# Kernel optimization log

Measured on AMD Instinct MI355X. Metric: run time of the kernel, lower is better.

The kernel has to match this reference:

```python
import jax, jax.numpy as jnp
import numpy as np

DIM = 384
HEADS = 8
HD = DIM // HEADS
GAMMA = 0.5
EPS = 1e-6
BN_EPS = 1e-5
LN_EPS = 1e-5


def setup_inputs() -> dict:
    key = jax.random.key(0)
    ks = jax.random.split(key, 8)
    B, H, W = 8, 56, 56
    d = DIM
    w = lambda k, shp: (jax.random.normal(k, shp, jnp.float32) * 0.05)
    return {
        "x": jax.random.normal(ks[0], (B, d, H, W), jnp.float32),
        "bn1_w": jnp.ones((d,), jnp.float32), "bn1_b": jnp.zeros((d,), jnp.float32),
        "bn1_m": jnp.zeros((d,), jnp.float32), "bn1_v": jnp.ones((d,), jnp.float32),
        "cw1": w(ks[1], (d, d)), "cb1": jnp.zeros((d,), jnp.float32),
        "dw": w(ks[2], (d, 1, 3, 3)), "db": jnp.zeros((d,), jnp.float32),
        "bn2_w": jnp.ones((d,), jnp.float32), "bn2_b": jnp.zeros((d,), jnp.float32),
        "bn2_m": jnp.zeros((d,), jnp.float32), "bn2_v": jnp.ones((d,), jnp.float32),
        "cw2": w(ks[3], (d, d)), "cb2": jnp.zeros((d,), jnp.float32),
        "qkv_w": w(ks[4], (3 * d, d)),
        "proj_w": w(ks[5], (d, d)), "proj_b": jnp.zeros((d,), jnp.float32),
        "ln_w": jnp.ones((d,), jnp.float32), "ln_b": jnp.zeros((d,), jnp.float32),
        "mlp_w1": w(ks[6], (d, 4 * d)), "mlp_b1": jnp.zeros((4 * d,), jnp.float32),
        "mlp_w2": w(ks[7], (4 * d, d)), "mlp_b2": jnp.zeros((d,), jnp.float32),
    }


def _bn(t, w, b, m, v):
    # inference-mode BatchNorm2d over channel dim of NCHW
    s = w * jax.lax.rsqrt(v + BN_EPS)
    return (t - m[:, None, None]) * s[:, None, None] + b[:, None, None]


def _c1(t, w, b=None):
    # 1x1 conv as channel GEMM: (o,i) x (b,i,h,w) -> (b,o,h,w)
    y = jnp.einsum('oi,bihw->bohw', w, t)
    return y if b is None else y + b[:, None, None]


def _phi(t):
    return jnp.exp(GAMMA * (2.0 * t - t * t))


def reference(x, bn1_w, bn1_b, bn1_m, bn1_v, cw1, cb1, dw, db,
              bn2_w, bn2_b, bn2_m, bn2_v, cw2, cb2, qkv_w,
              proj_w, proj_b, ln_w, ln_b, mlp_w1, mlp_b1, mlp_w2, mlp_b2):
    B, C, H, W = x.shape
    N = H * W
    # conv_path with residual
    h = _bn(x, bn1_w, bn1_b, bn1_m, bn1_v)
    h = _c1(h, cw1, cb1)
    h = jax.lax.conv_general_dilated(h, dw, (1, 1), 'SAME',
                                     feature_group_count=DIM,
                                     dimension_numbers=('NCHW', 'OIHW', 'NCHW'))
    h = h + db[:, None, None]
    h = _bn(h, bn2_w, bn2_b, bn2_m, bn2_v)
    h = _c1(h, cw2, cb2)
    x1 = h + x
    # linear attention
    qkv = _c1(x1, qkv_w)  # (B, 3C, H, W)
    q, k, v = jnp.split(qkv, 3, axis=1)
    to_heads = lambda t: t.reshape(B, HEADS, HD, N).transpose(0, 1, 3, 2)  # (B,h,N,d)
    qp = _phi(to_heads(q))
    kp = _phi(to_heads(k))
    vv = to_heads(v)
    kv = jnp.einsum('bhnd,bhne->bhde', kp, vv)               # (B,h,d,d)
    z = 1.0 / (jnp.einsum('bhnd,bhd->bhn', qp, kp.sum(axis=2)) + EPS)
    out = jnp.einsum('bhnd,bhde->bhne', qp, kv) * z[..., None]  # (B,h,N,d)
    out = out.transpose(0, 1, 3, 2).reshape(B, C, H, W)
    out = _c1(out, proj_w, proj_b)
    x2 = x1 + out
    # LayerNorm + MLP over channels
    xf = x2.transpose(0, 2, 3, 1)  # (B,H,W,C)
    mu = xf.mean(-1, keepdims=True)
    var = xf.var(-1, keepdims=True)
    xn = (xf - mu) * jax.lax.rsqrt(var + LN_EPS) * ln_w + ln_b
    hmid = jax.nn.gelu(xn @ mlp_w1 + mlp_b1, approximate=False)
    mlp_out = hmid @ mlp_w2 + mlp_b2
    return x2 + mlp_out.transpose(0, 3, 1, 2)
```

## Files before the change

### kernel.cpp

```cpp
#include <hip/hip_runtime.h>

#define CDIM 384
#define NPIX 3136
#define BB 8
#define NROW (BB * NPIX)
#define HDIM 48
#define CMID 1536
#define BN_EPS 1e-5f
#define LN_EPS 1e-5f

typedef short s16x8 __attribute__((ext_vector_type(8)));
typedef float f32x4 __attribute__((ext_vector_type(4)));
typedef unsigned short u16;

__device__ __forceinline__ u16 f2bf(float f) {
    unsigned u = __builtin_bit_cast(unsigned, f);
    u = (u + 0x7FFFu + ((u >> 16) & 1u)) >> 16;
    return (u16)u;
}
__device__ __forceinline__ float bf2f(u16 h) {
    unsigned u = ((unsigned)h) << 16;
    return __builtin_bit_cast(float, u);
}
__device__ __forceinline__ float phi_act(float v) { return expf(0.5f * (2.f * v - v * v)); }
__device__ __forceinline__ float gelu_act(float v) { return 0.5f * v * (1.f + erff(v * 0.7071067811865476f)); }

#define GLL16(g, l) __builtin_amdgcn_global_load_lds( \
    (const __attribute__((address_space(1))) void*)(g), \
    (__attribute__((address_space(3))) void*)(l), 16, 0, 0)

template<int ACT, bool BIAS, bool RES, bool OBF, bool OF32, int TN, bool QKV>
__global__ __launch_bounds__(256) void gemm_mfma(
    const u16* __restrict__ A, const u16* __restrict__ Bw,
    u16* __restrict__ Cbf, u16* __restrict__ Cv, float* __restrict__ Cf,
    const float* __restrict__ res, const float* __restrict__ bias,
    int N, int K)
{
    constexpr int NFR = TN / 32;
    constexpr int TNw = TN / 2;
    constexpr int STR = TNw + 4;
    constexpr int KLOOP_U16 = 8192 + TN * 64;
    constexpr int STG_U16 = 4 * 64 * STR;
    constexpr int SMEM_N = KLOOP_U16 > STG_U16 ? KLOOP_U16 : STG_U16;
    __shared__ __align__(16) u16 smem[SMEM_N];
    u16* Asb = smem;
    u16* Bsb = smem + 8192;

    const int t  = threadIdx.x;
    const int wv = t >> 6, ln = t & 63;
    const int lm = ln & 15, lq = ln >> 4;
    const int wm = wv >> 1, wn = wv & 1;
    const int m0 = blockIdx.y << 7, n0 = blockIdx.x * TN;

    const u16* gA0 = A  + (long)(m0 + wv * 16 + lm) * K + lq * 8;
    const u16* gA1 = gA0 + (long)64 * K;
    const u16* gB0 = Bw + (long)(n0 + wv * 16 + lm) * K + lq * 8;
    const u16* gB1 = gB0 + (long)64 * K;

    f32x4 acc[4][NFR] = {};
    const int nk = K >> 5;

    GLL16(gA0, &Asb[wv * 512]);
    GLL16(gA1, &Asb[wv * 512 + 2048]);
    GLL16(gB0, &Bsb[wv * 512]);
    if constexpr (TN == 128) GLL16(gB1, &Bsb[wv * 512 + 2048]);

    for (int k = 0; k < nk; k++) {
        const int cur = k & 1;
        __syncthreads();
        if (k + 1 < nk) {
            const int nx = cur ^ 1;
            gA0 += 32; gA1 += 32; gB0 += 32;
            GLL16(gA0, &Asb[nx * 4096 + wv * 512]);
            GLL16(gA1, &Asb[nx * 4096 + wv * 512 + 2048]);
            GLL16(gB0, &Bsb[nx * TN * 32 + wv * 512]);
            if constexpr (TN == 128) { gB1 += 32; GLL16(gB1, &Bsb[nx * TN * 32 + wv * 512 + 2048]); }
        }
        s16x8 av[4], bv[NFR];
        #pragma unroll
        for (int mf = 0; mf < 4; mf++)
            av[mf] = *(const s16x8*)&Asb[cur * 4096 + (wm * 256 + mf * 64 + ln) * 8];
        #pragma unroll
        for (int nf = 0; nf < NFR; nf++)
            bv[nf] = *(const s16x8*)&Bsb[cur * TN * 32 + ((TN == 128 ? wn * 256 : wn * 128) + nf * 64 + ln) * 8];
        #pragma unroll
        for (int mf = 0; mf < 4; mf++)
            #pragma unroll
            for (int nf = 0; nf < NFR; nf++)
                acc[mf][nf] = __builtin_amdgcn_mfma_f32_16x16x32_bf16(
                    av[mf], bv[nf], acc[mf][nf], 0, 0, 0);
    }

    u16* obase = Cbf; int oldc = N; int ocol0 = n0;
    bool qk_phi = false;
    if constexpr (QKV) {
        if (n0 < 768) { obase = Cbf; oldc = 768; ocol0 = n0; qk_phi = true; }
        else          { obase = Cv;  oldc = 384; ocol0 = n0 - 768; }
    }

    if constexpr (OBF || QKV) {
        __syncthreads();
        u16* stg = smem + wv * (64 * STR);
        #pragma unroll
        for (int nf = 0; nf < NFR; nf++) {
            const int lc = nf * 16 + lm;
            const int gn = n0 + wn * TNw + lc;
            const float bval = BIAS ? bias[gn] : 0.f;
            #pragma unroll
            for (int mf = 0; mf < 4; mf++) {
                #pragma unroll
                for (int r = 0; r < 4; r++) {
                    const int lr = mf * 16 + lq * 4 + r;
                    float v = acc[mf][nf][r];
                    if (BIAS) v += bval;
                    if (ACT == 1) v = phi_act(v);
                    else if (ACT == 2) v = gelu_act(v);
                    if (QKV) { if (qk_phi) v = phi_act(v); }
                    const long off = (long)(m0 + wm * 64 + lr) * N + gn;
                    if (RES) v += res[off];
                    if (OF32) Cf[off] = v;
                    stg[lr * STR + lc] = f2bf(v);
                }
            }
        }
        __syncthreads();
        constexpr int CPR = TNw / 8;
        constexpr int RPI = 64 / CPR;
        const int cg = ln % CPR, rb = ln / CPR;
        #pragma unroll
        for (int it = 0; it < 64 / RPI; it++) {
            const int row = it * RPI + rb;
            const s16x8 vv = *(const s16x8*)&stg[row * STR + cg * 8];
            *(s16x8*)&obase[(long)(m0 + wm * 64 + row) * oldc + ocol0 + wn * TNw + cg * 8] = vv;
        }
    } else {
        #pragma unroll
        for (int nf = 0; nf < NFR; nf++) {
            const int gn = n0 + wn * TNw + nf * 16 + lm;
            const float bval = BIAS ? bias[gn] : 0.f;
            #pragma unroll
            for (int mf = 0; mf < 4; mf++) {
                const int gmb = m0 + wm * 64 + mf * 16 + lq * 4;
                #pragma unroll
                for (int r = 0; r < 4; r++) {
                    float v = acc[mf][nf][r];
                    if (BIAS) v += bval;
                    if (ACT == 1) v = phi_act(v);
                    else if (ACT == 2) v = gelu_act(v);
                    const long off = (long)(gmb + r) * N + gn;
                    if (RES) v += res[off];
                    Cf[off] = v;
                }
            }
        }
    }
}

__global__ __launch_bounds__(256) void nchw_to_nhwc(const float* __restrict__ x,
                                                    float* __restrict__ of,
                                                    u16* __restrict__ ob)
{
    __shared__ float tile[64 * 65];
    const int n0 = blockIdx.x << 6, c0 = blockIdx.y << 6, b = blockIdx.z;
    const int t = threadIdx.x;
    const float* ip = x + ((long)b * CDIM + c0) * NPIX + n0;
    for (int idx = t; idx < 4096; idx += 256) {
        const int cc = idx >> 6, nn = idx & 63;
        tile[cc * 65 + nn] = ip[(long)cc * NPIX + nn];
    }
    __syncthreads();
    for (int idx = t; idx < 4096; idx += 256) {
        const int nn = idx >> 6, cc = idx & 63;
        const float v = tile[cc * 65 + nn];
        const long o = ((long)b * NPIX + n0 + nn) * CDIM + c0 + cc;
        of[o] = v; ob[o] = f2bf(v);
    }
}

__global__ __launch_bounds__(256) void dwconv_nhwc(const u16* __restrict__ in,
                                                   const u16* __restrict__ wt,
                                                   u16* __restrict__ out)
{
    const long tid = (long)blockIdx.x * 256 + threadIdx.x;
    const int c8 = (int)(tid % 48);
    const int p  = (int)((tid / 48) % NPIX);
    const int b  = (int)(tid / (48LL * NPIX));
    const int y = p / 56, x = p % 56;
    const u16* base = in + (long)b * NPIX * CDIM + c8 * 8;
    float acc[8] = {};
    #pragma unroll
    for (int r = 0; r < 3; r++) {
        const int yy = y + r - 1;
        if ((unsigned)yy >= 56u) continue;
        #pragma unroll
        for (int s = 0; s < 3; s++) {
            const int xx = x + s - 1;
            if ((unsigned)xx >= 56u) continue;
            const s16x8 iv = *(const s16x8*)&base[(long)(yy * 56 + xx) * CDIM];
            const s16x8 wv = *(const s16x8*)&wt[(r * 3 + s) * CDIM + c8 * 8];
            #pragma unroll
            for (int j = 0; j < 8; j++)
                acc[j] = fmaf(bf2f((u16)iv[j]), bf2f((u16)wv[j]), acc[j]);
        }
    }
    s16x8 ov;
    #pragma unroll
    for (int j = 0; j < 8; j++) ov[j] = (short)f2bf(acc[j]);
    *(s16x8*)&out[((long)b * NPIX + p) * CDIM + c8 * 8] = ov;
}

__global__ __launch_bounds__(256) void attn_kv_m(const u16* __restrict__ qk,
                                                 const u16* __restrict__ vb,
                                                 float* __restrict__ kv,
                                                 float* __restrict__ ksum)
{
    const int sp = blockIdx.x, bh = blockIdx.y;
    const int b = bh >> 3, h = bh & 7;
    const u16* kbase = qk + (long)b * NPIX * 768 + 384 + h * HDIM;
    const u16* vbase = vb + (long)b * NPIX * CDIM + h * HDIM;
    __shared__ u16 kt[48 * 72];
    __shared__ u16 vt[48 * 72];
    const int t = threadIdx.x;
    const int wv = t >> 6, ln = t & 63, lm = ln & 15, lq = ln >> 4;

    f32x4 acc[3] = {};
    const s16x8 ones = {0x3F80, 0x3F80, 0x3F80, 0x3F80, 0x3F80, 0x3F80, 0x3F80, 0x3F80};

    for (int tl = sp; tl < 49; tl += 8) {
        const int nn0 = tl << 6;
        __syncthreads();
        for (int idx = t; idx < 384; idx += 256) {
            const int oct = idx >> 6, nn = idx & 63;
            const s16x8 kvv = *(const s16x8*)&kbase[(long)(nn0 + nn) * 768 + oct * 8];
            const s16x8 vvv = *(const s16x8*)&vbase[(long)(nn0 + nn) * CDIM + oct * 8];
            #pragma unroll
            for (int j = 0; j < 8; j++) {
                kt[(oct * 8 + j) * 72 + nn] = (u16)kvv[j];
                vt[(oct * 8 + j) * 72 + nn] = (u16)vvv[j];
            }
        }
        __syncthreads();
        #pragma unroll
        for (int s = 0; s < 2; s++) {
            if (wv < 3) {
                const s16x8 av = *(const s16x8*)&kt[(wv * 16 + lm) * 72 + s * 32 + lq * 8];
                #pragma unroll
                for (int ef = 0; ef < 3; ef++) {
                    const s16x8 bv = *(const s16x8*)&vt[(ef * 16 + lm) * 72 + s * 32 + lq * 8];
                    acc[ef] = __builtin_amdgcn_mfma_f32_16x16x32_bf16(av, bv, acc[ef], 0, 0, 0);
                }
            } else {
                #pragma unroll
                for (int mf = 0; mf < 3; mf++) {
                    const s16x8 av = *(const s16x8*)&kt[(mf * 16 + lm) * 72 + s * 32 + lq * 8];
                    acc[mf] = __builtin_amdgcn_mfma_f32_16x16x32_bf16(av, ones, acc[mf], 0, 0, 0);
                }
            }
        }
    }
    if (wv < 3) {
        #pragma unroll
        for (int ef = 0; ef < 3; ef++)
            #pragma unroll
            for (int r = 0; r < 4; r++)
                atomicAdd(&kv[(long)bh * 2304 + (wv * 16 + lq * 4 + r) * 48 + ef * 16 + lm], acc[ef][r]);
    } else {
        if (lm == 0) {
            #pragma unroll
            for (int mf = 0; mf < 3; mf++)
                #pragma unroll
                for (int r = 0; r < 4; r++)
                    atomicAdd(&ksum[bh * 48 + mf * 16 + lq * 4 + r], acc[mf][r]);
        }
    }
}

__global__ void repack_kv(const float* __restrict__ kvb, const float* __restrict__ ksb,
                          u16* __restrict__ kvp, u16* __restrict__ ksp)
{
    const int bh = blockIdx.x, t = threadIdx.x;
    for (int idx = t; idx < 3072; idx += 256) {
        const int e = idx >> 6, d = idx & 63;
        kvp[(long)bh * 3072 + idx] = (d < 48) ? f2bf(kvb[(long)bh * 2304 + d * 48 + e]) : (u16)0;
    }
    if (t < 64) ksp[bh * 64 + t] = (t < 48) ? f2bf(ksb[bh * 48 + t]) : (u16)0;
}

__global__ __launch_bounds__(256) void attn_out_m(const u16* __restrict__ qk,
                                                  const u16* __restrict__ kvp,
                                                  const u16* __restrict__ ksp,
                                                  u16* __restrict__ outb)
{
    __shared__ __align__(16) u16 smem[4 * 7168];
    const int mt = blockIdx.x, hh = blockIdx.y, b = blockIdx.z;
    const int t = threadIdx.x, wv = t >> 6, ln = t & 63, lm = ln & 15, lq = ln >> 4;
    const int h = hh * 4 + wv, bh = b * 8 + h;
    u16* As = smem + wv * 7168;
    u16* Bs = As + 4096;
    const u16* Ab = qk + ((long)b * NPIX + mt * 64) * 768 + h * HDIM;
    const u16* Bb = kvp + (long)bh * 3072;

    #pragma unroll
    for (int rg = 0; rg < 4; rg++)
        #pragma unroll
        for (int oh = 0; oh < 2; oh++)
            GLL16(Ab + (long)(rg * 16 + lm) * 768 + oh * 32 + lq * 8, As + (rg * 128 + oh * 64) * 8);
    #pragma unroll
    for (int rg = 0; rg < 3; rg++)
        #pragma unroll
        for (int oh = 0; oh < 2; oh++)
            GLL16(Bb + (rg * 16 + lm) * 64 + oh * 32 + lq * 8, Bs + (rg * 128 + oh * 64) * 8);

    s16x8 kz[2];
    kz[0] = *(const s16x8*)&ksp[bh * 64 + lq * 8];
    kz[1] = *(const s16x8*)&ksp[bh * 64 + 32 + lq * 8];

    __syncthreads();

    f32x4 acc[4][3] = {};
    f32x4 accz[4] = {};
    #pragma unroll
    for (int s = 0; s < 2; s++) {
        s16x8 av[4], bv[3];
        #pragma unroll
        for (int mf = 0; mf < 4; mf++)
            av[mf] = *(const s16x8*)&As[(mf * 128 + s * 64 + ln) * 8];
        #pragma unroll
        for (int nf = 0; nf < 3; nf++)
            bv[nf] = *(const s16x8*)&Bs[(nf * 128 + s * 64 + ln) * 8];
        #pragma unroll
        for (int mf = 0; mf < 4; mf++) {
            #pragma unroll
            for (int nf = 0; nf < 3; nf++)
                acc[mf][nf] = __builtin_amdgcn_mfma_f32_16x16x32_bf16(av[mf], bv[nf], acc[mf][nf], 0, 0, 0);
            accz[mf] = __builtin_amdgcn_mfma_f32_16x16x32_bf16(av[mf], kz[s], accz[mf], 0, 0, 0);
        }
    }

    u16* stg = As;
    #pragma unroll
    for (int mf = 0; mf < 4; mf++) {
        #pragma unroll
        for (int r = 0; r < 4; r++) {
            const float z = 1.f / (accz[mf][r] + 1e-6f);
            const int row = mf * 16 + lq * 4 + r;
            #pragma unroll
            for (int nf = 0; nf < 3; nf++)
                stg[row * 56 + nf * 16 + lm] = f2bf(acc[mf][nf][r] * z);
        }
    }
    __syncthreads();

    #pragma unroll
    for (int it = 0; it < 6; it++) {
        const int idx = it * 256 + t;
        const int row = idx / 24, c = idx % 24;
        const int sw = c / 6, c6 = c % 6;
        const s16x8 vvv = *(const s16x8*)&smem[sw * 7168 + row * 56 + c6 * 8];
        *(s16x8*)&outb[((long)b * NPIX + mt * 64 + row) * CDIM + hh * 192 + c * 8] = vvv;
    }
}

__global__ __launch_bounds__(256) void ln_k(const float* __restrict__ x2,
                                            const float* __restrict__ lw,
                                            const float* __restrict__ lb,
                                            u16* __restrict__ xn)
{
    const int row = blockIdx.x * 4 + (threadIdx.x >> 6);
    const int lane = threadIdx.x & 63;
    const float* rp = x2 + (long)row * CDIM;
    float2 v[3];
    float sum = 0.f, sq = 0.f;
    #pragma unroll
    for (int i = 0; i < 3; i++) {
        v[i] = *(const float2*)&rp[lane * 2 + i * 128];
        sum += v[i].x + v[i].y;
        sq = fmaf(v[i].x, v[i].x, fmaf(v[i].y, v[i].y, sq));
    }
    #pragma unroll
    for (int off = 1; off < 64; off <<= 1) {
        sum += __shfl_xor(sum, off);
        sq  += __shfl_xor(sq, off);
    }
    const float mu = sum * (1.f / CDIM);
    const float rs = rsqrtf(sq * (1.f / CDIM) - mu * mu + LN_EPS);
    u16* op = xn + (long)row * CDIM;
    #pragma unroll
    for (int i = 0; i < 3; i++) {
        const int c = lane * 2 + i * 128;
        op[c]     = f2bf((v[i].x - mu) * rs * lw[c] + lb[c]);
        op[c + 1] = f2bf((v[i].y - mu) * rs * lw[c + 1] + lb[c + 1]);
    }
}

__global__ __launch_bounds__(256) void final_out(const float* __restrict__ x2,
                                                 const float* __restrict__ mlp,
                                                 float* __restrict__ out)
{
    __shared__ float tile[64 * 65];
    const int n0 = blockIdx.x << 6, c0 = blockIdx.y << 6, b = blockIdx.z;
    const int t = threadIdx.x;
    for (int idx = t; idx < 4096; idx += 256) {
        const int nn = idx >> 6, cc = idx & 63;
        const long o = ((long)b * NPIX + n0 + nn) * CDIM + c0 + cc;
        tile[nn * 65 + cc] = x2[o] + mlp[o];
    }
    __syncthreads();
    float* op = out + ((long)b * CDIM + c0) * NPIX + n0;
    for (int idx = t; idx < 4096; idx += 256) {
        const int cc = idx >> 6, nn = idx & 63;
        op[(long)cc * NPIX + nn] = tile[nn * 65 + cc];
    }
}

__global__ void prep_bn_k(const float* __restrict__ w1, const float* __restrict__ b1,
                          const float* __restrict__ m1, const float* __restrict__ v1,
                          const float* __restrict__ w2, const float* __restrict__ b2,
                          const float* __restrict__ m2, const float* __restrict__ v2,
                          const float* __restrict__ db,
                          float* s1, float* t1, float* s2, float* t2)
{
    const int i = threadIdx.x;
    if (i < CDIM) {
        const float a = w1[i] * rsqrtf(v1[i] + BN_EPS);
        s1[i] = a; t1[i] = b1[i] - m1[i] * a;
        const float c = w2[i] * rsqrtf(v2[i] + BN_EPS);
        s2[i] = c; t2[i] = b2[i] - m2[i] * c + db[i] * c;
    }
}

__global__ __launch_bounds__(64) void prep_w_k(
    const float* __restrict__ cw1, const float* __restrict__ cb1,
    const float* __restrict__ cw2, const float* __restrict__ cb2,
    const float* __restrict__ s1, const float* __restrict__ t1,
    const float* __restrict__ s2, const float* __restrict__ t2,
    u16* __restrict__ w1e, float* __restrict__ b1e,
    u16* __restrict__ w2e, float* __restrict__ b2e)
{
    const int o = blockIdx.x;
    const bool sec = (o >= CDIM);
    const int oo = sec ? o - CDIM : o;
    const float* cw = sec ? cw2 : cw1;
    const float* cb = sec ? cb2 : cb1;
    const float* s  = sec ? s2  : s1;
    const float* tt = sec ? t2  : t1;
    u16* we = sec ? w2e : w1e;
    float* be = sec ? b2e : b1e;
    float part = 0.f;
    for (int i = threadIdx.x; i < CDIM; i += 64) {
        const float wv = cw[oo * CDIM + i];
        we[oo * CDIM + i] = f2bf(wv * s[i]);
        part += wv * tt[i];
    }
    for (int off = 32; off; off >>= 1) part += __shfl_down(part, off);
    if (threadIdx.x == 0) be[oo] = cb[oo] + part;
}

__global__ void cvt_k(const float* __restrict__ in, u16* __restrict__ out, int n)
{
    const int i = blockIdx.x * 256 + threadIdx.x;
    if (i < n) out[i] = f2bf(in[i]);
}

__global__ __launch_bounds__(256) void transcvt_k(const float* __restrict__ in,
                                                  u16* __restrict__ out, int R, int C)
{
    __shared__ float tile[64 * 65];
    const int c0 = blockIdx.x << 6, r0 = blockIdx.y << 6;
    const int t = threadIdx.x;
    for (int idx = t; idx < 4096; idx += 256) {
        const int rr = idx >> 6, cc = idx & 63;
        tile[rr * 65 + cc] = in[(long)(r0 + rr) * C + c0 + cc];
    }
    __syncthreads();
    for (int idx = t; idx < 4096; idx += 256) {
        const int cc = idx >> 6, rr = idx & 63;
        out[(long)(c0 + cc) * R + r0 + rr] = f2bf(tile[rr * 65 + cc]);
    }
}

__global__ void dwt_k(const float* __restrict__ dw, u16* __restrict__ o)
{
    const int i = blockIdx.x * 256 + threadIdx.x;
    if (i < 9 * CDIM) {
        const int c = i / 9, tap = i % 9;
        o[tap * CDIM + c] = f2bf(dw[i]);
    }
}

extern "C" void kernel_launch(void* const* d_in, const int* in_sizes, int n_in,
                              void* d_out, int out_size, void* d_ws, size_t ws_size,
                              hipStream_t stream)
{
    const float* x      = (const float*)d_in[0];
    const float* bn1_w  = (const float*)d_in[1];
    const float* bn1_b  = (const float*)d_in[2];
    const float* bn1_m  = (const float*)d_in[3];
    const float* bn1_v  = (const float*)d_in[4];
    const float* cw1    = (const float*)d_in[5];
    const float* cb1    = (const float*)d_in[6];
    const float* dwW    = (const float*)d_in[7];
    const float* db     = (const float*)d_in[8];
    const float* bn2_w  = (const float*)d_in[9];
    const float* bn2_b  = (const float*)d_in[10];
    const float* bn2_m  = (const float*)d_in[11];
    const float* bn2_v  = (const float*)d_in[12];
    const float* cw2    = (const float*)d_in[13];
    const float* cb2    = (const float*)d_in[14];
    const float* qkv_w  = (const float*)d_in[15];
    const float* proj_w = (const float*)d_in[16];
    const float* proj_b = (const float*)d_in[17];
    const float* ln_w   = (const float*)d_in[18];
    const float* ln_b   = (const float*)d_in[19];
    const float* mlp_w1 = (const float*)d_in[20];
    const float* mlp_b1 = (const float*)d_in[21];
    const float* mlp_w2 = (const float*)d_in[22];
    const float* mlp_b2 = (const float*)d_in[23];
    float* outF = (float*)d_out;

    const long S = (long)NROW * CDIM;
    float* wsf = (float*)d_ws;

    float* xh_f  = wsf;
    float* x2_f  = wsf;
    u16*   v_bf  = (u16*)wsf;
    float* x1_f  = wsf + S;
    u16*   hmid  = (u16*)(wsf + S);
    u16* ar   = (u16*)(wsf + 2 * S);
    u16* a0   = ar;
    u16* a1   = ar + S;
    u16* a2   = ar + 2 * S;
    float* mlp_f = (float*)(ar + S);
    u16* wtb   = (u16*)(wsf + 3 * S + S / 2);
    u16* w1e   = wtb;
    u16* w2e   = w1e + CDIM * CDIM;
    u16* qkvw  = w2e + CDIM * CDIM;
    u16* projw = qkvw + 1152 * CDIM;
    u16* mw1t  = projw + CDIM * CDIM;
    u16* mw2t  = mw1t + CMID * CDIM;
    u16* dwt   = mw2t + CDIM * CMID;
    float* fb  = (float*)(dwt + 9 * CDIM);
    float* b1e = fb;
    float* b2e = b1e + CDIM;
    float* s1  = b2e + CDIM;
    float* t1  = s1 + CDIM;
    float* s2  = t1 + CDIM;
    float* t2  = s2 + CDIM;
    float* kvb = t2 + CDIM;
    float* ksb = kvb + 64 * HDIM * HDIM;
    u16*   kvp = (u16*)(ksb + 64 * HDIM);
    u16*   ksp = kvp + 64 * 3072;

    prep_bn_k<<<1, CDIM, 0, stream>>>(bn1_w, bn1_b, bn1_m, bn1_v,
                                      bn2_w, bn2_b, bn2_m, bn2_v, db, s1, t1, s2, t2);
    prep_w_k<<<2 * CDIM, 64, 0, stream>>>(cw1, cb1, cw2, cb2, s1, t1, s2, t2,
                                          w1e, b1e, w2e, b2e);
    cvt_k<<<(1152 * CDIM + 255) / 256, 256, 0, stream>>>(qkv_w, qkvw, 1152 * CDIM);
    cvt_k<<<(CDIM * CDIM + 255) / 256, 256, 0, stream>>>(proj_w, projw, CDIM * CDIM);
    transcvt_k<<<dim3(CMID / 64, CDIM / 64), 256, 0, stream>>>(mlp_w1, mw1t, CDIM, CMID);
    transcvt_k<<<dim3(CDIM / 64, CMID / 64), 256, 0, stream>>>(mlp_w2, mw2t, CMID, CDIM);
    dwt_k<<<(9 * CDIM + 255) / 256, 256, 0, stream>>>(dwW, dwt);

    nchw_to_nhwc<<<dim3(49, 6, 8), 256, 0, stream>>>(x, xh_f, a0);
    gemm_mfma<0, true, false, true, false, 64, false><<<dim3(6, 196), 256, 0, stream>>>(
        a0, w1e, a1, nullptr, nullptr, nullptr, b1e, CDIM, CDIM);
    dwconv_nhwc<<<(int)((long)BB * NPIX * 48 / 256), 256, 0, stream>>>(a1, dwt, a2);
    gemm_mfma<0, true, true, true, true, 64, false><<<dim3(6, 196), 256, 0, stream>>>(
        a2, w2e, a0, nullptr, x1_f, xh_f, b2e, CDIM, CDIM);
    gemm_mfma<0, false, false, true, false, 128, true><<<dim3(9, 196), 256, 0, stream>>>(
        a0, qkvw, a1, v_bf, nullptr, nullptr, nullptr, 1152, CDIM);
    hipMemsetAsync(kvb, 0, (size_t)(64 * HDIM * HDIM + 64 * HDIM) * sizeof(float), stream);
    attn_kv_m<<<dim3(8, 64), 256, 0, stream>>>(a1, v_bf, kvb, ksb);
    repack_kv<<<64, 256, 0, stream>>>(kvb, ksb, kvp, ksp);
    attn_out_m<<<dim3(49, 2, 8), 256, 0, stream>>>(a1, kvp, ksp, a0);
    gemm_mfma<0, true, true, false, true, 64, false><<<dim3(6, 196), 256, 0, stream>>>(
        a0, projw, nullptr, nullptr, x2_f, x1_f, proj_b, CDIM, CDIM);
    ln_k<<<NROW / 4, 256, 0, stream>>>(x2_f, ln_w, ln_b, a0);
    const long RH = (long)NROW / 2;
    gemm_mfma<2, true, false, true, false, 128, false><<<dim3(12, 98), 256, 0, stream>>>(
        a0, mw1t, hmid, nullptr, nullptr, nullptr, mlp_b1, CMID, CDIM);
    gemm_mfma<0, true, false, false, true, 64, false><<<dim3(6, 98), 256, 0, stream>>>(
        hmid, mw2t, nullptr, nullptr, mlp_f, nullptr, mlp_b2, CDIM, CMID);
    gemm_mfma<2, true, false, true, false, 128, false><<<dim3(12, 98), 256, 0, stream>>>(
        a0 + RH * CDIM, mw1t, hmid, nullptr, nullptr, nullptr, mlp_b1, CMID, CDIM);
    gemm_mfma<0, true, false, false, true, 64, false><<<dim3(6, 98), 256, 0, stream>>>(
        hmid, mw2t, nullptr, nullptr, mlp_f + RH * CDIM, nullptr, mlp_b2, CDIM, CMID);
    final_out<<<dim3(49, 6, 8), 256, 0, stream>>>(x2_f, mlp_f, outF);
}
```

Baseline: 623.5 us.

## Fuse final NCHW transpose into MLP GEMM epilogue and drop fp32 input copy

The second MLP GEMM now adds the x2 residual itself and writes straight into the NCHW output through an LDS-staged transpose, which removes the separate final_out kernel and the fp32 mlp intermediate buffer. The input conversion no longer writes an fp32 NHWC copy of x. The conv-path residual now reads the bf16 copy of x, which lowers the precision of that residual add. A block-index remap also groups consecutive tiles onto the same XCD to improve cache locality.

```diff
diff --git a/kernel.cpp b/kernel.cpp
--- a/kernel.cpp
+++ b/kernel.cpp
@@ -29,28 +29,37 @@
     (const __attribute__((address_space(1))) void*)(g), \
     (__attribute__((address_space(3))) void*)(l), 16, 0, 0)
 
-template<int ACT, bool BIAS, bool RES, bool OBF, bool OF32, int TN, bool QKV>
+template<int ACT, bool BIAS, int RES, bool OBF, bool OF32, bool ONCHW, int TN, bool QKV>
 __global__ __launch_bounds__(256) void gemm_mfma(
     const u16* __restrict__ A, const u16* __restrict__ Bw,
     u16* __restrict__ Cbf, u16* __restrict__ Cv, float* __restrict__ Cf,
-    const float* __restrict__ res, const float* __restrict__ bias,
-    int N, int K)
+    const void* __restrict__ resv, const float* __restrict__ bias,
+    int N, int K, long mrow0)
 {
     constexpr int NFR = TN / 32;
     constexpr int TNw = TN / 2;
     constexpr int STR = TNw + 4;
     constexpr int KLOOP_U16 = 8192 + TN * 64;
     constexpr int STG_U16 = 4 * 64 * STR;
-    constexpr int SMEM_N = KLOOP_U16 > STG_U16 ? KLOOP_U16 : STG_U16;
+    constexpr int ONCHW_U16 = ONCHW ? (64 * 132 * 2) : 0;
+    constexpr int SMEM_A = KLOOP_U16 > STG_U16 ? KLOOP_U16 : STG_U16;
+    constexpr int SMEM_N = SMEM_A > ONCHW_U16 ? SMEM_A : ONCHW_U16;
     __shared__ __align__(16) u16 smem[SMEM_N];
     u16* Asb = smem;
     u16* Bsb = smem + 8192;
+
+    const int total = gridDim.x * gridDim.y;
+    const int flat = blockIdx.y * gridDim.x + blockIdx.x;
+    const int nx8 = total >> 3, rem = total & 7;
+    const int xcd = flat & 7, slot = flat >> 3;
+    const int nf2 = xcd * nx8 + (xcd < rem ? xcd : rem) + slot;
+    const int by = nf2 / gridDim.x, bx = nf2 - by * gridDim.x;
 
     const int t  = threadIdx.x;
     const int wv = t >> 6, ln = t & 63;
     const int lm = ln & 15, lq = ln >> 4;
     const int wm = wv >> 1, wn = wv & 1;
-    const int m0 = blockIdx.y << 7, n0 = blockIdx.x * TN;
+    const int m0 = by << 7, n0 = bx * TN;
 
     const u16* gA0 = A  + (long)(m0 + wv * 16 + lm) * K + lq * 8;
     const u16* gA1 = gA0 + (long)64 * K;
@@ -117,7 +126,8 @@
                     else if (ACT == 2) v = gelu_act(v);
                     if (QKV) { if (qk_phi) v = phi_act(v); }
                     const long off = (long)(m0 + wm * 64 + lr) * N + gn;
-                    if (RES) v += res[off];
+                    if (RES == 1) v += ((const float*)resv)[off];
+                    else if (RES == 2) v += bf2f(((const u16*)resv)[off]);
                     if (OF32) Cf[off] = v;
                     stg[lr * STR + lc] = f2bf(v);
                 }
@@ -132,6 +142,44 @@
             const int row = it * RPI + rb;
             const s16x8 vv = *(const s16x8*)&stg[row * STR + cg * 8];
             *(s16x8*)&obase[(long)(m0 + wm * 64 + row) * oldc + ocol0 + wn * TNw + cg * 8] = vv;
+        }
+    } else if constexpr (ONCHW) {
+        __syncthreads();
+        float* stgf = (float*)smem;
+        const float* resf = (const float*)resv;
+        #pragma unroll
+        for (int nf = 0; nf < NFR; nf++) {
+            const int lc = nf * 16 + lm;
+            const int col = wn * TNw + lc;
+            const int gn = n0 + col;
+            const float bval = BIAS ? bias[gn] : 0.f;
+            #pragma unroll
+            for (int mf = 0; mf < 4; mf++) {
+                float4 q;
+                float* qq = (float*)&q;
+                #pragma unroll
+                for (int r = 0; r < 4; r++) {
+                    const int lr = mf * 16 + lq * 4 + r;
+                    float v = acc[mf][nf][r];
+                    if (BIAS) v += bval;
+                    if (ACT == 1) v = phi_act(v);
+                    else if (ACT == 2) v = gelu_act(v);
+                    if (RES == 1) v += resf[(long)(m0 + wm * 64 + lr) * N + gn];
+                    qq[r] = v;
+                }
+                *(float4*)&stgf[col * 132 + wm * 64 + mf * 16 + lq * 4] = q;
+            }
+        }
+        __syncthreads();
+        #pragma unroll
+        for (int it = 0; it < 8; it++) {
+            const int c = it * 8 + (t >> 5);
+            const int mloc = (t & 31) * 4;
+            const float4 vv = *(const float4*)&stgf[c * 132 + mloc];
+            const long mg = mrow0 + m0 + mloc;
+            const int b = (int)(mg / NPIX);
+            const int n = (int)(mg % NPIX);
+            *(float4*)&Cf[((long)b * CDIM + n0 + c) * NPIX + n] = vv;
         }
     } else {
         #pragma unroll
@@ -148,7 +196,8 @@
                     if (ACT == 1) v = phi_act(v);
                     else if (ACT == 2) v = gelu_act(v);
                     const long off = (long)(gmb + r) * N + gn;
-                    if (RES) v += res[off];
+                    if (RES == 1) v += ((const float*)resv)[off];
+                    else if (RES == 2) v += bf2f(((const u16*)resv)[off]);
                     Cf[off] = v;
                 }
             }
@@ -156,9 +205,8 @@
     }
 }
 
-__global__ __launch_bounds__(256) void nchw_to_nhwc(const float* __restrict__ x,
-                                                    float* __restrict__ of,
-                                                    u16* __restrict__ ob)
+__global__ __launch_bounds__(256) void nchw_to_bf(const float* __restrict__ x,
+                                                  u16* __restrict__ ob)
 {
     __shared__ float tile[64 * 65];
     const int n0 = blockIdx.x << 6, c0 = blockIdx.y << 6, b = blockIdx.z;
@@ -171,9 +219,7 @@
     __syncthreads();
     for (int idx = t; idx < 4096; idx += 256) {
         const int nn = idx >> 6, cc = idx & 63;
-        const float v = tile[cc * 65 + nn];
-        const long o = ((long)b * NPIX + n0 + nn) * CDIM + c0 + cc;
-        of[o] = v; ob[o] = f2bf(v);
+        ob[((long)b * NPIX + n0 + nn) * CDIM + c0 + cc] = f2bf(tile[cc * 65 + nn]);
     }
 }
 
@@ -390,26 +436,6 @@
         const int c = lane * 2 + i * 128;
         op[c]     = f2bf((v[i].x - mu) * rs * lw[c] + lb[c]);
         op[c + 1] = f2bf((v[i].y - mu) * rs * lw[c + 1] + lb[c + 1]);
-    }
-}
-
-__global__ __launch_bounds__(256) void final_out(const float* __restrict__ x2,
-                                                 const float* __restrict__ mlp,
-                                                 float* __restrict__ out)
-{
-    __shared__ float tile[64 * 65];
-    const int n0 = blockIdx.x << 6, c0 = blockIdx.y << 6, b = blockIdx.z;
-    const int t = threadIdx.x;
-    for (int idx = t; idx < 4096; idx += 256) {
-        const int nn = idx >> 6, cc = idx & 63;
-        const long o = ((long)b * NPIX + n0 + nn) * CDIM + c0 + cc;
-        tile[nn * 65 + cc] = x2[o] + mlp[o];
-    }
-    __syncthreads();
-    float* op = out + ((long)b * CDIM + c0) * NPIX + n0;
-    for (int idx = t; idx < 4096; idx += 256) {
-        const int cc = idx >> 6, nn = idx & 63;
-        op[(long)cc * NPIX + nn] = tile[nn * 65 + cc];
     }
 }
 
@@ -521,7 +547,6 @@
     const long S = (long)NROW * CDIM;
     float* wsf = (float*)d_ws;
 
-    float* xh_f  = wsf;
     float* x2_f  = wsf;
     u16*   v_bf  = (u16*)wsf;
     float* x1_f  = wsf + S;
@@ -530,7 +555,6 @@
     u16* a0   = ar;
     u16* a1   = ar + S;
     u16* a2   = ar + 2 * S;
-    float* mlp_f = (float*)(ar + S);
     u16* wtb   = (u16*)(wsf + 3 * S + S / 2);
     u16* w1e   = wtb;
     u16* w2e   = w1e + CDIM * CDIM;
@@ -561,29 +585,28 @@
     transcvt_k<<<dim3(CDIM / 64, CMID / 64), 256, 0, stream>>>(mlp_w2, mw2t, CMID, CDIM);
     dwt_k<<<(9 * CDIM + 255) / 256, 256, 0, stream>>>(dwW, dwt);
 
-    nchw_to_nhwc<<<dim3(49, 6, 8), 256, 0, stream>>>(x, xh_f, a0);
-    gemm_mfma<0, true, false, true, false, 64, false><<<dim3(6, 196), 256, 0, stream>>>(
-        a0, w1e, a1, nullptr, nullptr, nullptr, b1e, CDIM, CDIM);
+    nchw_to_bf<<<dim3(49, 6, 8), 256, 0, stream>>>(x, a0);
+    gemm_mfma<0, true, 0, true, false, false, 64, false><<<dim3(6, 196), 256, 0, stream>>>(
+        a0, w1e, a1, nullptr, nullptr, nullptr, b1e, CDIM, CDIM, 0);
     dwconv_nhwc<<<(int)((long)BB * NPIX * 48 / 256), 256, 0, stream>>>(a1, dwt, a2);
-    gemm_mfma<0, true, true, true, true, 64, false><<<dim3(6, 196), 256, 0, stream>>>(
-        a2, w2e, a0, nullptr, x1_f, xh_f, b2e, CDIM, CDIM);
-    gemm_mfma<0, false, false, true, false, 128, true><<<dim3(9, 196), 256, 0, stream>>>(
-        a0, qkvw, a1, v_bf, nullptr, nullptr, nullptr, 1152, CDIM);
+    gemm_mfma<0, true, 2, true, true, false, 64, false><<<dim3(6, 196), 256, 0, stream>>>(
+        a2, w2e, a0, nullptr, x1_f, a0, b2e, CDIM, CDIM, 0);
+    gemm_mfma<0, false, 0, true, false, false, 128, true><<<dim3(9, 196), 256, 0, stream>>>(
+        a0, qkvw, a1, v_bf, nullptr, nullptr, nullptr, 1152, CDIM, 0);
     hipMemsetAsync(kvb, 0, (size_t)(64 * HDIM * HDIM + 64 * HDIM) * sizeof(float), stream);
     attn_kv_m<<<dim3(8, 64), 256, 0, stream>>>(a1, v_bf, kvb, ksb);
     repack_kv<<<64, 256, 0, stream>>>(kvb, ksb, kvp, ksp);
     attn_out_m<<<dim3(49, 2, 8), 256, 0, stream>>>(a1, kvp, ksp, a0);
-    gemm_mfma<0, true, true, false, true, 64, false><<<dim3(6, 196), 256, 0, stream>>>(
-        a0, projw, nullptr, nullptr, x2_f, x1_f, proj_b, CDIM, CDIM);
+    gemm_mfma<0, true, 1, false, true, false, 64, false><<<dim3(6, 196), 256, 0, stream>>>(
+        a0, projw, nullptr, nullptr, x2_f, x1_f, proj_b, CDIM, CDIM, 0);
     ln_k<<<NROW / 4, 256, 0, stream>>>(x2_f, ln_w, ln_b, a0);
     const long RH = (long)NROW / 2;
-    gemm_mfma<2, true, false, true, false, 128, false><<<dim3(12, 98), 256, 0, stream>>>(
-        a0, mw1t, hmid, nullptr, nullptr, nullptr, mlp_b1, CMID, CDIM);
-    gemm_mfma<0, true, false, false, true, 64, false><<<dim3(6, 98), 256, 0, stream>>>(
-        hmid, mw2t, nullptr, nullptr, mlp_f, nullptr, mlp_b2, CDIM, CMID);
-    gemm_mfma<2, true, false, true, false, 128, false><<<dim3(12, 98), 256, 0, stream>>>(
-        a0 + RH * CDIM, mw1t, hmid, nullptr, nullptr, nullptr, mlp_b1, CMID, CDIM);
-    gemm_mfma<0, true, false, false, true, 64, false><<<dim3(6, 98), 256, 0, stream>>>(
-        hmid, mw2t, nullptr, nullptr, mlp_f + RH * CDIM, nullptr, mlp_b2, CDIM, CMID);
-    final_out<<<dim3(49, 6, 8), 256, 0, stream>>>(x2_f, mlp_f, outF);
-}
+    gemm_mfma<2, true, 0, true, false, false, 128, false><<<dim3(12, 98), 256, 0, stream>>>(
+        a0, mw1t, hmid, nullptr, nullptr, nullptr, mlp_b1, CMID, CDIM, 0);
+    gemm_mfma<0, true, 1, false, false, true, 64, false><<<dim3(6, 98), 256, 0, stream>>>(
+        hmid, mw2t, nullptr, nullptr, outF, x2_f, mlp_b2, CDIM, CMID, 0);
+    gemm_mfma<2, true, 0, true, false, false, 128, false><<<dim3(12, 98), 256, 0, stream>>>(
+        a0 + RH * CDIM, mw1t, hmid, nullptr, nullptr, nullptr, mlp_b1, CMID, CDIM, 0);
+    gemm_mfma<0, true, 1, false, false, true, 64, false><<<dim3(6, 98), 256, 0, stream>>>(
+        hmid, mw2t, nullptr, nullptr, outF, x2_f + RH * CDIM, mlp_b2, CDIM, CMID, RH);
+}
```

Result: faster. 566.2 us (-9.2%).
